# Kernel optimization log

Measured on AMD Instinct MI355X. Metric: run time of the kernel, lower is better.

The kernel has to match this reference:

```python
import jax, jax.numpy as jnp
import numpy as np
from jax.scipy.special import logsumexp

B, T, F = 32, 256, 32   # batch, line width (time), line height (features)
HID = 128
VOCAB = 100             # blank index = VOCAB
LBL = 32                # label length
NEG = -1e30


def _mdlstm(x, Wx, Wh1, Wh2, b):
    # x: [B, H, W, C] -> 2D LSTM: outer scan over width, inner scan over height
    Bb, H, W, C = x.shape
    hid = Wh1.shape[0]

    def col_step(carry, x_col):
        c_left, h_left = carry  # [H, B, hid] states from previous column

        def row_step(rc, inp):
            c_up, h_up = rc          # [B, hid] from previous row
            x_ij, c_l, h_l = inp     # [B, C], [B, hid], [B, hid]
            z = x_ij @ Wx + h_l @ Wh1 + h_up @ Wh2 + b  # [B, 5*hid]
            i_, g_, f1, f2, o_ = jnp.split(z, 5, axis=-1)
            c = jax.nn.sigmoid(f1) * c_l + jax.nn.sigmoid(f2) * c_up + jax.nn.sigmoid(i_) * jnp.tanh(g_)
            h = jax.nn.sigmoid(o_) * jnp.tanh(c)
            return (c, h), (c, h)

        z0 = jnp.zeros((Bb, hid), x.dtype)
        _, (c_col, h_col) = jax.lax.scan(row_step, (z0, z0), (x_col, c_left, h_left))
        return (c_col, h_col), h_col

    x_t = jnp.transpose(x, (2, 1, 0, 3))  # [W, H, B, C]
    zc = jnp.zeros((H, Bb, hid), x.dtype)
    _, hs = jax.lax.scan(col_step, (zc, zc), x_t)  # [W, H, B, hid]
    return jnp.transpose(hs, (2, 1, 0, 3))  # [B, H, W, hid]


def _ctc_loss(logp, labels, blank):
    # logp: [B, T, V] log-softmax; labels: [B, L] int in [0, blank)
    Bb, Tt, V = logp.shape
    Ll = labels.shape[1]
    S = 2 * Ll + 1
    ext = jnp.full((Bb, S), blank, dtype=labels.dtype).at[:, 1::2].set(labels)  # blank-interleaved
    lp_ext = jnp.take_along_axis(logp, jnp.broadcast_to(ext[:, None, :], (Bb, Tt, S)), axis=2)  # [B,T,S]
    prev2 = jnp.concatenate([jnp.full((Bb, 2), blank, dtype=ext.dtype), ext[:, :-2]], axis=1)
    skip = (ext != blank) & (ext != prev2)
    skip = skip.at[:, :2].set(False)
    alpha0 = jnp.full((Bb, S), NEG, logp.dtype).at[:, 0].set(lp_ext[:, 0, 0]).at[:, 1].set(lp_ext[:, 0, 1])

    def step(alpha, lp_t):
        a1 = jnp.concatenate([jnp.full((Bb, 1), NEG, alpha.dtype), alpha[:, :-1]], axis=1)
        a2 = jnp.concatenate([jnp.full((Bb, 2), NEG, alpha.dtype), alpha[:, :-2]], axis=1)
        a2 = jnp.where(skip, a2, NEG)
        new = logsumexp(jnp.stack([alpha, a1, a2], axis=0), axis=0) + lp_t
        return new, None

    alphaT, _ = jax.lax.scan(step, alpha0, jnp.transpose(lp_ext, (1, 0, 2))[1:])
    ll = logsumexp(jnp.stack([alphaT[:, -1], alphaT[:, -2]], axis=0), axis=0)
    return -ll  # [B]


def setup_inputs() -> dict:
    key = jax.random.key(0)
    ks = jax.random.split(key, 8)
    s = 0.08
    return {
        "X": jax.random.normal(ks[0], (B, T, F), jnp.float32),
        "y": jax.random.randint(ks[1], (B, LBL), 0, VOCAB),
        "Wx": jax.random.normal(ks[2], (1, 5 * HID), jnp.float32) * s,
        "Wh1": jax.random.normal(ks[3], (HID, 5 * HID), jnp.float32) * s,
        "Wh2": jax.random.normal(ks[4], (HID, 5 * HID), jnp.float32) * s,
        "b": jax.random.normal(ks[5], (5 * HID,), jnp.float32) * 0.01,
        "W_fc": jax.random.normal(ks[6], (HID, VOCAB + 1), jnp.float32) * s,
        "b_fc": jax.random.normal(ks[7], (VOCAB + 1,), jnp.float32) * 0.01,
    }


def reference(X, y, Wx, Wh1, Wh2, b, W_fc, b_fc):
    x = jnp.transpose(X, (0, 2, 1))[..., None]        # [B, F, T, 1] (image)
    h = _mdlstm(x, Wx, Wh1, Wh2, b)                    # [B, F, T, HID]
    feat = jnp.sum(h, axis=1)                          # collapse over height -> [B, T, HID]
    logits = feat @ W_fc + b_fc                        # [B, T, VOCAB+1]
    logp = jax.nn.log_softmax(logits, axis=-1)
    return _ctc_loss(logp, y, VOCAB)                   # per-example CTC loss [B]
```

## Files before the change

kernel.cpp:

```cpp
#include <hip/hip_runtime.h>

#define NEGF (-1e30f)

typedef __attribute__((ext_vector_type(8))) short short8;
typedef __attribute__((ext_vector_type(4))) float float4v;

template <bool V> struct BC { static constexpr bool value = V; };

__device__ __forceinline__ short f2bf(float f) {
  union { float f; unsigned u; } v; v.f = f;
  unsigned r = v.u + 0x7fffu + ((v.u >> 16) & 1u);
  return (short)(r >> 16);
}
__device__ __forceinline__ float fastrcp(float x) { return __builtin_amdgcn_rcpf(x); }
__device__ __forceinline__ float clamp15(float x) { return fminf(15.0f, fmaxf(-15.0f, x)); }

__global__ void prep_w_kernel(const float* __restrict__ Wh1, const float* __restrict__ Wh2,
                              short* __restrict__ wsW) {
  int t = blockIdx.x * 256 + threadIdx.x;
  int lane = t & 63;
  int frag = t >> 6;
  int nt = frag >> 3, kk = frag & 7;
  int n  = nt * 16 + (lane & 15);
  int kb = kk * 32 + (lane >> 4) * 8;
  short8 v;
#pragma unroll
  for (int j = 0; j < 8; ++j) {
    int k = kb + j;
    float w = (k < 128) ? Wh1[k * 640 + n] : Wh2[(k - 128) * 640 + n];
    v[j] = f2bf(w);
  }
  ((short8*)wsW)[frag * 64 + lane] = v;
}

__global__ __launch_bounds__(512)
void mdlstm_kernel(const float* __restrict__ X, const short* __restrict__ wsW,
                   const float* __restrict__ Wx, const float* __restrict__ bias,
                   float* __restrict__ feat) {
  __shared__ __align__(16) short h_buf[2][33][136];
  __shared__ __align__(16) short wlds[14 * 4096];
  __shared__ float featbuf[33][132];

  const int bat  = blockIdx.x;
  const int tid  = threadIdx.x;
  const int lane = tid & 63;
  const int g    = tid >> 6;
  const int col  = lane & 15;
  const int quad = lane >> 4;
  const int jj   = g * 16 + col;

  for (int i = tid; i < 4488; i += 512) ((int*)h_buf)[i] = 0;
  for (int i = tid; i < 33 * 132; i += 512) ((float*)featbuf)[i] = 0.0f;
  {
    const uint4* s4 = (const uint4*)wsW;
    uint4* d4 = (uint4*)wlds;
    for (int i = tid; i < 14 * 512; i += 512) {
      int c = i >> 9, off = i & 511;
      int gg = off >> 6, ln = off & 63;
      int q  = (c < 7) ? 3 : 4;
      int kk = (c < 7) ? c : (c - 7);
      d4[i] = s4[(((q * 8 + gg) * 8) + kk) * 64 + ln];
    }
  }

  float wx[5], bg[5];
#pragma unroll
  for (int q = 0; q < 5; ++q) {
    wx[q] = Wx[q * 128 + jj];
    bg[q] = bias[q * 128 + jj];
  }

  const short8* W8 = (const short8*)wsW;
  short8 rb0[8], rb1[8], rb2[8];
#pragma unroll
  for (int kk = 0; kk < 8; ++kk) {
    rb0[kk] = W8[((0 * 8 + g) * 8 + kk) * 64 + lane];
    rb1[kk] = W8[((1 * 8 + g) * 8 + kk) * 64 + lane];
    rb2[kk] = W8[((2 * 8 + g) * 8 + kk) * 64 + lane];
  }
  const short8 rb37 = W8[((3 * 8 + g) * 8 + 7) * 64 + lane];
  const short8 rb47 = W8[((4 * 8 + g) * 8 + 7) * 64 + lane];

  const short8* pL3 = (const short8*)wlds + g * 64 + lane;
  const short8* pL4 = (const short8*)wlds + 7 * 512 + g * 64 + lane;

  float cp0[4] = {0.f, 0.f, 0.f, 0.f};
  float cp1[4] = {0.f, 0.f, 0.f, 0.f};
  const float* Xb = X + bat * 8192;
  float* fb = feat + bat * 32768;

  int sb = 0;
  __syncthreads();

  auto stepT = [&](int d, auto allv_) {
    constexpr bool ALLV = decltype(allv_)::value;
    const int rbuf = (d + 1) & 1, wbuf = d & 1;

    if (d >= 32 && tid < 128) {
      int fs = sb + 1; if (fs >= 33) fs = 0;
      float v = featbuf[fs][tid];
      featbuf[fs][tid] = 0.0f;
      fb[(d - 32) * 128 + tid] = v;
    }

    float4v acc0[5], acc1[5];
#pragma unroll
    for (int q = 0; q < 5; ++q) {
      acc0[q] = (float4v){bg[q], bg[q], bg[q], bg[q]};
      acc1[q] = acc0[q];
    }
#pragma unroll
    for (int kk = 0; kk < 8; ++kk) {
      const int up = kk >> 2;
      const int ccc = (kk & 3) * 32 + quad * 8;
      short8 a0 = *(const short8*)&h_buf[rbuf][col + 1 - up][ccc];
      short8 a1 = *(const short8*)&h_buf[rbuf][17 + col - up][ccc];
      short8 b3 = (kk < 7) ? pL3[kk * 512] : rb37;
      acc0[3] = __builtin_amdgcn_mfma_f32_16x16x32_bf16(a0, b3, acc0[3], 0, 0, 0);
      acc1[3] = __builtin_amdgcn_mfma_f32_16x16x32_bf16(a1, b3, acc1[3], 0, 0, 0);
      short8 b4 = (kk < 7) ? pL4[kk * 512] : rb47;
      acc0[4] = __builtin_amdgcn_mfma_f32_16x16x32_bf16(a0, b4, acc0[4], 0, 0, 0);
      acc1[4] = __builtin_amdgcn_mfma_f32_16x16x32_bf16(a1, b4, acc1[4], 0, 0, 0);
      short8 b0 = rb0[kk];
      acc0[0] = __builtin_amdgcn_mfma_f32_16x16x32_bf16(a0, b0, acc0[0], 0, 0, 0);
      acc1[0] = __builtin_amdgcn_mfma_f32_16x16x32_bf16(a1, b0, acc1[0], 0, 0, 0);
      short8 b1 = rb1[kk];
      acc0[1] = __builtin_amdgcn_mfma_f32_16x16x32_bf16(a0, b1, acc0[1], 0, 0, 0);
      acc1[1] = __builtin_amdgcn_mfma_f32_16x16x32_bf16(a1, b1, acc1[1], 0, 0, 0);
      short8 b2 = rb2[kk];
      acc0[2] = __builtin_amdgcn_mfma_f32_16x16x32_bf16(a0, b2, acc0[2], 0, 0, 0);
      acc1[2] = __builtin_amdgcn_mfma_f32_16x16x32_bf16(a1, b2, acc1[2], 0, 0, 0);
    }

    float t00 = __shfl_up(cp0[3], 16);
    float t10 = __shfl_up(cp1[3], 16);
    float c15 = __shfl(cp0[3], 48 + col);
    float cu0[4], cu1[4];
    cu0[0] = quad ? t00 : 0.0f; cu0[1] = cp0[0]; cu0[2] = cp0[1]; cu0[3] = cp0[2];
    cu1[0] = quad ? t10 : c15;  cu1[1] = cp1[0]; cu1[2] = cp1[1]; cu1[3] = cp1[2];

    auto halfc = [&](float4v (&acc)[5], float (&cp)[4], float (&cu)[4], int mbase) {
#pragma unroll
      for (int r = 0; r < 4; ++r) {
        const int m = mbase + r;
        const int w = d - m;
        if (ALLV || (unsigned)w < 256u) {
          const float x = Xb[w * 32 + m];
          float zi = clamp15(fmaf(x, wx[0], acc[0][r]));
          float zg = clamp15(fmaf(x, wx[1], acc[1][r]));
          float z1 = clamp15(fmaf(x, wx[2], acc[2][r]));
          float z2 = clamp15(fmaf(x, wx[3], acc[3][r]));
          float zo = clamp15(fmaf(x, wx[4], acc[4][r]));
          float e1 = __expf(z1), e2 = __expf(z2), ei = __expf(zi), eg = __expf(2.0f * zg);
          float A1 = 1.0f + e1, A2 = 1.0f + e2, Ai = 1.0f + ei, G = 1.0f + eg;
          float P = Ai * G, Q = A1 * A2;
          float rD = fastrcp(P * Q);
          float c = (e1 * cp[r] * (A2 * P) + e2 * cu[r] * (A1 * P) + ei * (eg - 1.0f) * Q) * rD;
          float eo = __expf(-zo);
          float ec = __expf(2.0f * clamp15(c));
          float h = (ec - 1.0f) * fastrcp((1.0f + eo) * (ec + 1.0f));
          cp[r] = c;
          h_buf[wbuf][1 + m][jj] = f2bf(h);
          int s = sb - m; if (s < 0) s += 33;
          featbuf[s][jj] += h;
        }
      }
    };
    halfc(acc0, cp0, cu0, quad * 4);
    halfc(acc1, cp1, cu1, 16 + quad * 4);
    __syncthreads();
  };

  BC<true> Tv; BC<false> Fv;
  for (int d = 0; d < 31; ++d)    { stepT(d, Fv); sb = (sb == 32) ? 0 : sb + 1; }
  for (int d = 31; d < 256; ++d)  { stepT(d, Tv); sb = (sb == 32) ? 0 : sb + 1; }
  for (int d = 256; d < 287; ++d) { stepT(d, Fv); sb = (sb == 32) ? 0 : sb + 1; }

  int fs = sb + 1; if (fs >= 33) fs = 0;
  if (tid < 128) fb[255 * 128 + tid] = featbuf[fs][tid];
}

__global__ __launch_bounds__(256)
void logits_kernel(const float* __restrict__ feat, const float* __restrict__ Wfc,
                   const float* __restrict__ bfc, float* __restrict__ logp) {
  __shared__ float sW[128 * 101];
  __shared__ float sF[8][128];
  __shared__ float sL[8][104];
  __shared__ float sLse[8];
  const int tid = threadIdx.x;
  const int b  = blockIdx.x >> 5;
  const int t0 = (blockIdx.x & 31) * 8;

  for (int i = tid; i < 128 * 101; i += 256) sW[i] = Wfc[i];
  for (int i = tid; i < 8 * 128; i += 256)
    sF[i >> 7][i & 127] = feat[(b * 256 + t0 + (i >> 7)) * 128 + (i & 127)];
  __syncthreads();
  for (int idx = tid; idx < 8 * 101; idx += 256) {
    int tr = idx / 101, v = idx - tr * 101;
    float s = bfc[v];
#pragma unroll 4
    for (int k = 0; k < 128; ++k) s += sF[tr][k] * sW[k * 101 + v];
    sL[tr][v] = s;
  }
  __syncthreads();
  if (tid < 8) {
    float m = NEGF;
    for (int v = 0; v < 101; ++v) m = fmaxf(m, sL[tid][v]);
    float su = 0.0f;
    for (int v = 0; v < 101; ++v) su += __expf(sL[tid][v] - m);
    sLse[tid] = m + __logf(su);
  }
  __syncthreads();
  for (int idx = tid; idx < 8 * 101; idx += 256) {
    int tr = idx / 101, v = idx - tr * 101;
    logp[(b * 256 + t0 + tr) * 101 + v] = sL[tr][v] - sLse[tr];
  }
}

__global__ __launch_bounds__(64)
void ctc_kernel(const float* __restrict__ logp, const int* __restrict__ y,
                float* __restrict__ out) {
  const int b = blockIdx.x;
  const int l = threadIdx.x;
  const float* lpb = logp + b * 256 * 101;
  const int* yb = y + b * 32;
  int lab = (l & 1) ? yb[l >> 1] : 100;
  bool skip = (l & 1) && (l >= 3) && (yb[l >> 1] != yb[(l >> 1) - 1]);

  float a   = (l == 0) ? lpb[100] : ((l == 1) ? lpb[lab] : NEGF);
  float a64 = NEGF;
  float pl[4], pb[4];
#pragma unroll
  for (int tt = 0; tt < 4; ++tt) {
    pl[tt] = lpb[(1 + tt) * 101 + lab];
    pb[tt] = lpb[(1 + tt) * 101 + 100];
  }
#pragma unroll 4
  for (int t = 1; t < 256; ++t) {
    const int s = (t - 1) & 3;
    float lpl = pl[s], lpbk = pb[s];
    if (t + 4 < 256) {
      pl[s] = lpb[(t + 4) * 101 + lab];
      pb[s] = lpb[(t + 4) * 101 + 100];
    }
    float am1 = __shfl_up(a, 1); if (l == 0) am1 = NEGF;
    float am2 = __shfl_up(a, 2); if (l < 2 || !skip) am2 = NEGF;
    float m3 = fmaxf(a, fmaxf(am1, am2));
    float na = m3 + __logf(__expf(a - m3) + __expf(am1 - m3) + __expf(am2 - m3)) + lpl;
    float m2 = fmaxf(a64, a);
    float na64 = m2 + __logf(__expf(a64 - m2) + __expf(a - m2)) + lpbk;
    a = na;
    a64 = na64;
  }
  float A63 = __shfl(a, 63);
  float A64 = __shfl(a64, 63);
  if (l == 0) {
    float m = fmaxf(A63, A64);
    out[b] = -(m + __logf(__expf(A63 - m) + __expf(A64 - m)));
  }
}

extern "C" void kernel_launch(void* const* d_in, const int* in_sizes, int n_in,
                              void* d_out, int out_size, void* d_ws, size_t ws_size,
                              hipStream_t stream) {
  const float* X   = (const float*)d_in[0];
  const int*   y   = (const int*)d_in[1];
  const float* Wx  = (const float*)d_in[2];
  const float* Wh1 = (const float*)d_in[3];
  const float* Wh2 = (const float*)d_in[4];
  const float* bi  = (const float*)d_in[5];
  const float* Wfc = (const float*)d_in[6];
  const float* bfc = (const float*)d_in[7];
  float* out = (float*)d_out;

  char* ws = (char*)d_ws;
  short* wsW  = (short*)(ws);
  float* logp = (float*)(ws + 0x50000);
  float* feat = (float*)(ws + 0x378000);

  hipMemsetAsync(feat, 0, 32 * 256 * 128 * sizeof(float), stream);
  prep_w_kernel<<<80, 256, 0, stream>>>(Wh1, Wh2, wsW);
  mdlstm_kernel<<<32, 512, 0, stream>>>(X, wsW, Wx, bi, feat);
  logits_kernel<<<1024, 256, 0, stream>>>(feat, Wfc, bfc, logp);
  ctc_kernel<<<32, 64, 0, stream>>>(logp, y, out);
}
```

Before: 1.080 ms.

## Split MDLSTM rows across two wave groups with 1024-thread blocks

Doubles the MDLSTM block to 1024 threads so each wave handles 16 rows instead of 32. The cell state at the boundary between the two row halves now passes through a shared-memory buffer instead of a shuffle. Register-resident weights for gates 0-2 are replaced by global/L2 loads inside the inner loop to cut register pressure. The change also uses fmed3 for clamping and drops the redundant memset of feat. Per-step latency should fall through more parallelism, at the cost of repeated weight loads from global memory every step.

```diff
diff --git a/kernel.cpp b/kernel.cpp
--- a/kernel.cpp
+++ b/kernel.cpp
@@ -13,7 +13,7 @@
   return (short)(r >> 16);
 }
 __device__ __forceinline__ float fastrcp(float x) { return __builtin_amdgcn_rcpf(x); }
-__device__ __forceinline__ float clamp15(float x) { return fminf(15.0f, fmaxf(-15.0f, x)); }
+__device__ __forceinline__ float clamp15(float x) { return __builtin_amdgcn_fmed3f(x, -15.0f, 15.0f); }
 
 __global__ void prep_w_kernel(const float* __restrict__ Wh1, const float* __restrict__ Wh2,
                               short* __restrict__ wsW) {
@@ -33,28 +33,32 @@
   ((short8*)wsW)[frag * 64 + lane] = v;
 }
 
-__global__ __launch_bounds__(512)
+__global__ __launch_bounds__(1024)
 void mdlstm_kernel(const float* __restrict__ X, const short* __restrict__ wsW,
                    const float* __restrict__ Wx, const float* __restrict__ bias,
                    float* __restrict__ feat) {
   __shared__ __align__(16) short h_buf[2][33][136];
   __shared__ __align__(16) short wlds[14 * 4096];
   __shared__ float featbuf[33][132];
+  __shared__ float c_bnd[2][132];
 
   const int bat  = blockIdx.x;
   const int tid  = threadIdx.x;
   const int lane = tid & 63;
-  const int g    = tid >> 6;
+  const int w    = tid >> 6;
+  const int half = w >> 3;
+  const int g    = w & 7;
   const int col  = lane & 15;
   const int quad = lane >> 4;
   const int jj   = g * 16 + col;
 
-  for (int i = tid; i < 4488; i += 512) ((int*)h_buf)[i] = 0;
-  for (int i = tid; i < 33 * 132; i += 512) ((float*)featbuf)[i] = 0.0f;
+  for (int i = tid; i < 4488; i += 1024) ((int*)h_buf)[i] = 0;
+  for (int i = tid; i < 33 * 132; i += 1024) ((float*)featbuf)[i] = 0.0f;
+  if (tid < 264) ((float*)c_bnd)[tid] = 0.0f;
   {
     const uint4* s4 = (const uint4*)wsW;
     uint4* d4 = (uint4*)wlds;
-    for (int i = tid; i < 14 * 512; i += 512) {
+    for (int i = tid; i < 14 * 512; i += 1024) {
       int c = i >> 9, off = i & 511;
       int gg = off >> 6, ln = off & 63;
       int q  = (c < 7) ? 3 : 4;
@@ -69,26 +73,22 @@
     wx[q] = Wx[q * 128 + jj];
     bg[q] = bias[q * 128 + jj];
   }
-
+  float cp[4] = {0.f, 0.f, 0.f, 0.f};
+
+  const float* Xb = X + bat * 8192;
+  float* fb = feat + bat * 32768;
   const short8* W8 = (const short8*)wsW;
-  short8 rb0[8], rb1[8], rb2[8];
-#pragma unroll
-  for (int kk = 0; kk < 8; ++kk) {
-    rb0[kk] = W8[((0 * 8 + g) * 8 + kk) * 64 + lane];
-    rb1[kk] = W8[((1 * 8 + g) * 8 + kk) * 64 + lane];
-    rb2[kk] = W8[((2 * 8 + g) * 8 + kk) * 64 + lane];
-  }
+  const short8* pW0 = W8 + ((0 * 8 + g) * 8) * 64 + lane;
+  const short8* pW1 = W8 + ((1 * 8 + g) * 8) * 64 + lane;
+  const short8* pW2 = W8 + ((2 * 8 + g) * 8) * 64 + lane;
   const short8 rb37 = W8[((3 * 8 + g) * 8 + 7) * 64 + lane];
   const short8 rb47 = W8[((4 * 8 + g) * 8 + 7) * 64 + lane];
-
   const short8* pL3 = (const short8*)wlds + g * 64 + lane;
   const short8* pL4 = (const short8*)wlds + 7 * 512 + g * 64 + lane;
 
-  float cp0[4] = {0.f, 0.f, 0.f, 0.f};
-  float cp1[4] = {0.f, 0.f, 0.f, 0.f};
-  const float* Xb = X + bat * 8192;
-  float* fb = feat + bat * 32768;
-
+  const int mbase  = half * 16 + quad * 4;
+  const int rowoff = 1 + half * 16;
+  const float* pX = Xb - 31 * mbase;
   int sb = 0;
   __syncthreads();
 
@@ -103,71 +103,67 @@
       fb[(d - 32) * 128 + tid] = v;
     }
 
-    float4v acc0[5], acc1[5];
-#pragma unroll
-    for (int q = 0; q < 5; ++q) {
-      acc0[q] = (float4v){bg[q], bg[q], bg[q], bg[q]};
-      acc1[q] = acc0[q];
-    }
+    float4v acc[5];
+#pragma unroll
+    for (int q = 0; q < 5; ++q) acc[q] = (float4v){bg[q], bg[q], bg[q], bg[q]};
 #pragma unroll
     for (int kk = 0; kk < 8; ++kk) {
-      const int up = kk >> 2;
-      const int ccc = (kk & 3) * 32 + quad * 8;
-      short8 a0 = *(const short8*)&h_buf[rbuf][col + 1 - up][ccc];
-      short8 a1 = *(const short8*)&h_buf[rbuf][17 + col - up][ccc];
+      const int up = (kk >= 4) ? 1 : 0;
+      const int cc = (kk & 3) * 32 + quad * 8;
+      short8 a0 = *(const short8*)&h_buf[rbuf][col + rowoff - up][cc];
       short8 b3 = (kk < 7) ? pL3[kk * 512] : rb37;
-      acc0[3] = __builtin_amdgcn_mfma_f32_16x16x32_bf16(a0, b3, acc0[3], 0, 0, 0);
-      acc1[3] = __builtin_amdgcn_mfma_f32_16x16x32_bf16(a1, b3, acc1[3], 0, 0, 0);
+      acc[3] = __builtin_amdgcn_mfma_f32_16x16x32_bf16(a0, b3, acc[3], 0, 0, 0);
       short8 b4 = (kk < 7) ? pL4[kk * 512] : rb47;
-      acc0[4] = __builtin_amdgcn_mfma_f32_16x16x32_bf16(a0, b4, acc0[4], 0, 0, 0);
-      acc1[4] = __builtin_amdgcn_mfma_f32_16x16x32_bf16(a1, b4, acc1[4], 0, 0, 0);
-      short8 b0 = rb0[kk];
-      acc0[0] = __builtin_amdgcn_mfma_f32_16x16x32_bf16(a0, b0, acc0[0], 0, 0, 0);
-      acc1[0] = __builtin_amdgcn_mfma_f32_16x16x32_bf16(a1, b0, acc1[0], 0, 0, 0);
-      short8 b1 = rb1[kk];
-      acc0[1] = __builtin_amdgcn_mfma_f32_16x16x32_bf16(a0, b1, acc0[1], 0, 0, 0);
-      acc1[1] = __builtin_amdgcn_mfma_f32_16x16x32_bf16(a1, b1, acc1[1], 0, 0, 0);
-      short8 b2 = rb2[kk];
-      acc0[2] = __builtin_amdgcn_mfma_f32_16x16x32_bf16(a0, b2, acc0[2], 0, 0, 0);
-      acc1[2] = __builtin_amdgcn_mfma_f32_16x16x32_bf16(a1, b2, acc1[2], 0, 0, 0);
-    }
-
-    float t00 = __shfl_up(cp0[3], 16);
-    float t10 = __shfl_up(cp1[3], 16);
-    float c15 = __shfl(cp0[3], 48 + col);
-    float cu0[4], cu1[4];
-    cu0[0] = quad ? t00 : 0.0f; cu0[1] = cp0[0]; cu0[2] = cp0[1]; cu0[3] = cp0[2];
-    cu1[0] = quad ? t10 : c15;  cu1[1] = cp1[0]; cu1[2] = cp1[1]; cu1[3] = cp1[2];
-
-    auto halfc = [&](float4v (&acc)[5], float (&cp)[4], float (&cu)[4], int mbase) {
-#pragma unroll
-      for (int r = 0; r < 4; ++r) {
-        const int m = mbase + r;
-        const int w = d - m;
-        if (ALLV || (unsigned)w < 256u) {
-          const float x = Xb[w * 32 + m];
-          float zi = clamp15(fmaf(x, wx[0], acc[0][r]));
-          float zg = clamp15(fmaf(x, wx[1], acc[1][r]));
-          float z1 = clamp15(fmaf(x, wx[2], acc[2][r]));
-          float z2 = clamp15(fmaf(x, wx[3], acc[3][r]));
-          float zo = clamp15(fmaf(x, wx[4], acc[4][r]));
-          float e1 = __expf(z1), e2 = __expf(z2), ei = __expf(zi), eg = __expf(2.0f * zg);
-          float A1 = 1.0f + e1, A2 = 1.0f + e2, Ai = 1.0f + ei, G = 1.0f + eg;
-          float P = Ai * G, Q = A1 * A2;
-          float rD = fastrcp(P * Q);
-          float c = (e1 * cp[r] * (A2 * P) + e2 * cu[r] * (A1 * P) + ei * (eg - 1.0f) * Q) * rD;
-          float eo = __expf(-zo);
-          float ec = __expf(2.0f * clamp15(c));
-          float h = (ec - 1.0f) * fastrcp((1.0f + eo) * (ec + 1.0f));
-          cp[r] = c;
-          h_buf[wbuf][1 + m][jj] = f2bf(h);
-          int s = sb - m; if (s < 0) s += 33;
-          featbuf[s][jj] += h;
-        }
+      acc[4] = __builtin_amdgcn_mfma_f32_16x16x32_bf16(a0, b4, acc[4], 0, 0, 0);
+      short8 b2 = pW2[kk * 64];
+      acc[2] = __builtin_amdgcn_mfma_f32_16x16x32_bf16(a0, b2, acc[2], 0, 0, 0);
+      short8 b0 = pW0[kk * 64];
+      acc[0] = __builtin_amdgcn_mfma_f32_16x16x32_bf16(a0, b0, acc[0], 0, 0, 0);
+      short8 b1 = pW1[kk * 64];
+      acc[1] = __builtin_amdgcn_mfma_f32_16x16x32_bf16(a0, b1, acc[1], 0, 0, 0);
+    }
+
+    float t0 = __shfl_up(cp[3], 16);
+    float c15 = c_bnd[rbuf][jj];
+    float cu[4];
+    cu[0] = quad ? t0 : (half ? c15 : 0.0f);
+    cu[1] = cp[0]; cu[2] = cp[1]; cu[3] = cp[2];
+    const float* pXd = pX + d * 32;
+    float xm[4];
+#pragma unroll
+    for (int r = 0; r < 4; ++r) {
+      int ww = d - (mbase + r);
+      if (ALLV || (ww >= 0 && ww < 256)) xm[r] = pXd[-31 * r];
+    }
+#pragma unroll
+    for (int r = 0; r < 4; ++r) {
+      const int m = mbase + r;
+      const int ww = d - m;
+      if (ALLV || (ww >= 0 && ww < 256)) {
+        float c_up = cu[r];
+        float c_l  = cp[r];
+        float x    = xm[r];
+        float zi = clamp15(fmaf(x, wx[0], acc[0][r]));
+        float zg = clamp15(fmaf(x, wx[1], acc[1][r]));
+        float z1 = clamp15(fmaf(x, wx[2], acc[2][r]));
+        float z2 = clamp15(fmaf(x, wx[3], acc[3][r]));
+        float zo = clamp15(fmaf(x, wx[4], acc[4][r]));
+        float e1 = __expf(z1), e2 = __expf(z2), ei = __expf(zi), eg = __expf(2.0f * zg);
+        float A1 = 1.0f + e1, A2 = 1.0f + e2, Ai = 1.0f + ei, G = 1.0f + eg;
+        float P = Ai * G, Q = A1 * A2;
+        float rD = fastrcp(P * Q);
+        float c = (e1 * c_l * (A2 * P) + e2 * c_up * (A1 * P) + ei * (eg - 1.0f) * Q) * rD;
+        float eo = __expf(-zo);
+        float ec = __expf(2.0f * clamp15(c));
+        float h = (ec - 1.0f) * fastrcp((1.0f + eo) * (ec + 1.0f));
+        cp[r] = c;
+        h_buf[wbuf][1 + m][jj] = f2bf(h);
+        int s = sb - m; if (s < 0) s += 33;
+        featbuf[s][jj] += h;
+        if (!half && r == 3 && quad == 3)
+          c_bnd[wbuf][jj] = c;
       }
-    };
-    halfc(acc0, cp0, cu0, quad * 4);
-    halfc(acc1, cp1, cu1, 16 + quad * 4);
+    }
     __syncthreads();
   };
 
@@ -278,9 +274,8 @@
   float* logp = (float*)(ws + 0x50000);
   float* feat = (float*)(ws + 0x378000);
 
-  hipMemsetAsync(feat, 0, 32 * 256 * 128 * sizeof(float), stream);
   prep_w_kernel<<<80, 256, 0, stream>>>(Wh1, Wh2, wsW);
-  mdlstm_kernel<<<32, 512, 0, stream>>>(X, wsW, Wx, bi, feat);
+  mdlstm_kernel<<<32, 1024, 0, stream>>>(X, wsW, Wx, bi, feat);
   logits_kernel<<<1024, 256, 0, stream>>>(feat, Wfc, bfc, logp);
   ctc_kernel<<<32, 64, 0, stream>>>(logp, y, out);
 }
```

Result: slower. 2.481 ms (+129.8%).
